# Kernel optimization log

Hardware: AMD Instinct MI355X
Metric: run time of the kernel (lower is better)

Reference implementation:

```python
import jax, jax.numpy as jnp
import numpy as np

NX, NY = 512, 512
DX, DY = 1e-4, 1e-4
VS = 1550.0
DT = 2.5e-8


def setup_inputs() -> dict:
    key = jax.random.key(0)
    k1, k2 = jax.random.split(key)
    sensor_data = jax.random.normal(k1, (4, 2, 128, 2048), dtype=jnp.float32)
    sensor_xy = jax.random.randint(k2, (128, 2), 0, 512, dtype=jnp.int32)
    return {"sensor_data": sensor_data, "sensor_xy": sensor_xy}


def _delay_indices(sensor_xy):
    # pixel grids, 1-indexed as in the torch code (arange(1,513))
    ix = jnp.arange(1, NX + 1, dtype=jnp.float32)[None, :, None]  # (1,Nx,1)
    iy = jnp.arange(1, NY + 1, dtype=jnp.float32)[None, None, :]  # (1,1,Ny)
    x = sensor_xy[:, 0].astype(jnp.float32)[:, None, None]        # (S,1,1)
    y = sensor_xy[:, 1].astype(jnp.float32)[:, None, None]
    dis = jnp.sqrt(((x - ix + 1.0) * DX) ** 2 + ((y - iy + 1.0) * DY) ** 2)  # (S,Nx,Ny)
    # .to(torch.long) truncates; values are non-negative so int cast matches
    return (dis / VS / DT).astype(jnp.int32).reshape(sensor_xy.shape[0], -1)  # (S, Nx*Ny)


def reference(sensor_data, sensor_xy):
    B = sensor_data.shape[0]
    S = sensor_xy.shape[0]
    t = _delay_indices(sensor_xy)                           # (S, P) int32
    data = jnp.transpose(sensor_data, (2, 0, 1, 3))         # (S, B, 2, T)

    def step(img, xs):
        t_s, d_s = xs                                       # (P,), (B,2,T)
        return img + d_s[:, :, t_s], None                   # gather + accumulate

    img0 = jnp.zeros((B, 2, NX * NY), dtype=sensor_data.dtype)
    img, _ = jax.lax.scan(step, img0, (t, data))
    return img.reshape(B, 2, NX, NY)
```

## Files before the change

kernel.cpp:

```cpp
#include <hip/hip_runtime.h>
#include <math.h>


#define NXY 512
#define S_CNT 128
#define T_CNT 2048
#define CH 8
#define CH_STRIDE (S_CNT * T_CNT)
#define NPIX (NXY * NXY)
#define TAB_BYTES (NPIX * 2)
#define CHUNK 32
#define NCHUNK (S_CNT / CHUNK)
#define PATW 24
#define PAT_ROW_B (PATW * 2)
#define PAT_SENS_B (16 * PAT_ROW_B)

typedef float f32x2 __attribute__((ext_vector_type(2)));

#if __has_builtin(__builtin_amdgcn_sad_u32)
__device__ __forceinline__ unsigned int sadu(unsigned int a, unsigned int b, unsigned int c) {
    return __builtin_amdgcn_sad_u32(a, b, c);
}
#else
__device__ __forceinline__ unsigned int sadu(unsigned int a, unsigned int b, unsigned int c) {
    return (a > b ? a - b : b - a) + c;
}
#endif

#pragma float_control(push)
#pragma float_control(precise, on)
__device__ __forceinline__ unsigned short delay_entry(int adx, int ady) {
    const double DX32 = (double)1e-4f;
    const double R1 = (double)(float)(1.0 / 1550.0);
    const double R2 = (double)(float)(1.0 / (double)2.5e-8f);
    float dxf = (float)((double)adx * DX32);
    float dyf = (float)((double)ady * DX32);
    float a2 = (float)((double)dxf * (double)dxf);
    float b2 = (float)((double)dyf * (double)dyf);
    float sum = (float)((double)a2 + (double)b2);
    float dis = (float)sqrt((double)sum);
    float q1 = (float)((double)dis * R1);
    float q2 = (float)((double)q1 * R2);
    return (unsigned short)(int)q2;
}

__device__ __forceinline__ unsigned int bf16_rne(float f) {
    unsigned int x = __float_as_uint(f);
    return (x + 0x7fffu + ((x >> 16) & 1u)) >> 16;
}

__global__ __launch_bounds__(256) void prep(const float* __restrict__ data,
                                            unsigned short* __restrict__ tab,
                                            uint4* __restrict__ d2b) {
    int idx = blockIdx.x * 256 + threadIdx.x;
    tab[idx] = (unsigned short)((unsigned int)delay_entry(idx >> 9, idx & 511) << 4);

    unsigned int w[4];
#pragma unroll
    for (int j = 0; j < 4; ++j) {
        unsigned int lo = bf16_rne(data[(2 * j) * CH_STRIDE + idx]);
        unsigned int hi = bf16_rne(data[(2 * j + 1) * CH_STRIDE + idx]);
        w[j] = lo | (hi << 16);
    }
    d2b[idx] = make_uint4(w[0], w[1], w[2], w[3]);
}
#pragma float_control(pop)

__device__ __forceinline__ float bflo(unsigned int u) { return __uint_as_float(u << 16); }
__device__ __forceinline__ float bfhi(unsigned int u) { return __uint_as_float(u & 0xffff0000u); }

__global__ __launch_bounds__(256) void das_sad(const uint4* __restrict__ d2b,
                                               const unsigned short* __restrict__ tab,
                                               const int* __restrict__ sxy,
                                               float* __restrict__ out) {
    __shared__ uint4 minfo[S_CNT];
    __shared__ unsigned int mstage[S_CNT];
    __shared__ uint4 patb[CHUNK * 16 * 3];

    int tid = threadIdx.x;
    int x0 = (blockIdx.x >> 5) << 4;
    int y0 = (blockIdx.x & 31) << 4;

    if (tid < S_CNT) {
        int sxv = sxy[2 * tid];
        int syv = sxy[2 * tid + 1];
        int axm = sxv < x0 ? x0 - sxv : (sxv > x0 + 15 ? sxv - x0 - 15 : 0);
        int aym = syv < y0 ? y0 - syv : (syv > y0 + 15 ? syv - y0 - 15 : 0);
        int ay0 = aym & ~7;
        minfo[tid] = make_uint4((unsigned int)sxv, (unsigned int)(2 * syv),
                                (unsigned int)(-(axm * 48 + ay0 * 2)), 0u);
        mstage[tid] = (unsigned int)(axm | (ay0 << 16));
    }
    __syncthreads();

    int iy = y0 | (((tid >> 6) & 1) << 3) | (tid & 7);
    int ix = x0 | ((tid >> 7) << 3) | ((tid >> 3) & 7);
    unsigned int uix = (unsigned int)ix;
    unsigned int uiy2 = (unsigned int)(2 * iy);

    f32x2 acc2[4];
#pragma unroll
    for (int k = 0; k < 4; ++k) acc2[k] = (f32x2){0.0f, 0.0f};

    const char* patc = (const char*)patb;

    for (int c = 0; c < NCHUNK; ++c) {
        int s0 = c * CHUNK;

#pragma unroll
        for (int j = 0; j < 6; ++j) {
            unsigned int idx = (unsigned int)tid + 256u * j;
            unsigned int r3 = idx / 3u;
            unsigned int cc = idx - r3 * 3u;
            unsigned int row = r3 & 15u;
            unsigned int ls = r3 >> 4;
            unsigned int st = mstage[s0 + ls];
            int ax0 = (int)(st & 0xffffu);
            int ay0 = (int)(st >> 16);
            const uint4* src = (const uint4*)((const char*)tab +
                (((size_t)(ax0 + (int)row) << 10) + ((size_t)ay0 << 1) + ((size_t)cc << 4)));
            patb[ls * 48u + row * 3u + cc] = *src;
        }
        __syncthreads();

        const char* d2bc = (const char*)d2b + ((size_t)s0 << 15);
#pragma unroll 8
        for (int ls = 0; ls < CHUNK; ++ls) {
            uint4 mi = minfo[s0 + ls];
            unsigned int b1 = sadu(mi.x, uix, 0u);
            unsigned int b2 = sadu(mi.y, uiy2, mi.z);
            unsigned int byte = b1 * 48u + b2;
            unsigned int t16 = (unsigned int)*(const unsigned short*)(
                patc + (size_t)(ls * PAT_SENS_B) + byte);
            uint4 w = *(const uint4*)(d2bc + ((size_t)ls << 15) + t16);
            f32x2 p0 = {bflo(w.x), bfhi(w.x)};
            f32x2 p1 = {bflo(w.y), bfhi(w.y)};
            f32x2 p2 = {bflo(w.z), bfhi(w.z)};
            f32x2 p3 = {bflo(w.w), bfhi(w.w)};
            acc2[0] += p0;
            acc2[1] += p1;
            acc2[2] += p2;
            acc2[3] += p3;
        }
        __syncthreads();
    }

    int pix = (ix << 9) | iy;
#pragma unroll
    for (int k = 0; k < 4; ++k) {
        out[(2 * k) * NPIX + pix] = acc2[k].x;
        out[(2 * k + 1) * NPIX + pix] = acc2[k].y;
    }
}

#pragma float_control(push)
#pragma float_control(precise, on)
__global__ __launch_bounds__(256) void build_table(unsigned short* __restrict__ tab) {
    int idx = blockIdx.x * 256 + threadIdx.x;
    tab[idx] = delay_entry(idx >> 9, idx & 511);
}
#pragma float_control(pop)

__global__ __launch_bounds__(256) void das_main(const float* __restrict__ data,
                                                const unsigned short* __restrict__ tab,
                                                const int* __restrict__ sxy,
                                                float* __restrict__ out) {
    __shared__ int sx[S_CNT];
    __shared__ int sy[S_CNT];
    int tid = threadIdx.x;
    if (tid < S_CNT) {
        sx[tid] = sxy[2 * tid];
        sy[tid] = sxy[2 * tid + 1];
    }
    __syncthreads();
    int iy = ((blockIdx.x & 31) << 4) | (tid & 15);
    int ix = ((blockIdx.x >> 5) << 4) | (tid >> 4);
    float acc[CH];
#pragma unroll
    for (int k = 0; k < CH; ++k) acc[k] = 0.0f;
#pragma unroll 4
    for (int s = 0; s < S_CNT; ++s) {
        int dxi = sx[s] - ix;
        int dyi = sy[s] - iy;
        int adx = dxi < 0 ? -dxi : dxi;
        int ady = dyi < 0 ? -dyi : dyi;
        int t = (int)tab[(adx << 9) | ady];
        const float* p = data + (s << 11) + t;
#pragma unroll
        for (int k = 0; k < CH; ++k) acc[k] += p[(size_t)k * CH_STRIDE];
    }
    int pix = (ix << 9) | iy;
#pragma unroll
    for (int k = 0; k < CH; ++k) out[k * NPIX + pix] = acc[k];
}

extern "C" void kernel_launch(void* const* d_in, const int* in_sizes, int n_in,
                              void* d_out, int out_size, void* d_ws, size_t ws_size,
                              hipStream_t stream) {
    const float* data = (const float*)d_in[0];
    const int* sxy = (const int*)d_in[1];
    float* out = (float*)d_out;
    unsigned short* tab = (unsigned short*)d_ws;

    size_t need = (size_t)TAB_BYTES + (size_t)CH_STRIDE * 16;
    if (ws_size >= need) {
        uint4* d2b = (uint4*)((char*)d_ws + TAB_BYTES);
        prep<<<NPIX / 256, 256, 0, stream>>>(data, tab, d2b);
        das_sad<<<1024, 256, 0, stream>>>(d2b, tab, sxy, out);
    } else {
        build_table<<<NPIX / 256, 256, 0, stream>>>(tab);
        das_main<<<1024, 256, 0, stream>>>(data, tab, sxy, out);
    }
}
```

Baseline: 111.6 us.

## Stage per-sensor time windows in LDS and gather from shared memory

For each 16x16 pixel tile and sensor, the kernel computes the minimum delay and copies a 64-sample window of packed bf16 data into shared memory. The delay pattern is rebased relative to that minimum and XOR-swizzled to reduce bank conflicts. The per-pixel gathers then read from LDS instead of global memory, with table lookups batched ahead of the loads. The chunk size drops from 32 to 8 sensors, which adds more barriers. The code assumes each tile's delay span fits within 64 samples, and the float_control precise pragmas around the delay computation are removed, which could change how the delay indices round.

```diff
diff --git a/kernel.cpp b/kernel.cpp
--- a/kernel.cpp
+++ b/kernel.cpp
@@ -9,8 +9,9 @@
 #define CH_STRIDE (S_CNT * T_CNT)
 #define NPIX (NXY * NXY)
 #define TAB_BYTES (NPIX * 2)
-#define CHUNK 32
+#define CHUNK 8
 #define NCHUNK (S_CNT / CHUNK)
+#define WIN 64
 #define PATW 24
 #define PAT_ROW_B (PATW * 2)
 #define PAT_SENS_B (16 * PAT_ROW_B)
@@ -27,8 +28,6 @@
 }
 #endif
 
-#pragma float_control(push)
-#pragma float_control(precise, on)
 __device__ __forceinline__ unsigned short delay_entry(int adx, int ady) {
     const double DX32 = (double)1e-4f;
     const double R1 = (double)(float)(1.0 / 1550.0);
@@ -64,17 +63,26 @@
     }
     d2b[idx] = make_uint4(w[0], w[1], w[2], w[3]);
 }
-#pragma float_control(pop)
 
 __device__ __forceinline__ float bflo(unsigned int u) { return __uint_as_float(u << 16); }
 __device__ __forceinline__ float bfhi(unsigned int u) { return __uint_as_float(u & 0xffff0000u); }
 
-__global__ __launch_bounds__(256) void das_sad(const uint4* __restrict__ d2b,
+__device__ __forceinline__ unsigned int swz16(unsigned int d) {
+    return d ^ (((d >> 7) & 3u) << 4);
+}
+__device__ __forceinline__ unsigned int subswz_x2(unsigned int a, unsigned int tm4) {
+    unsigned int lo = swz16((a - tm4) & 0xffffu);
+    unsigned int hi = swz16(((a >> 16) - tm4) & 0xffffu);
+    return lo | (hi << 16);
+}
+
+__global__ __launch_bounds__(256) void das_win(const uint4* __restrict__ d2b,
                                                const unsigned short* __restrict__ tab,
                                                const int* __restrict__ sxy,
                                                float* __restrict__ out) {
     __shared__ uint4 minfo[S_CNT];
-    __shared__ unsigned int mstage[S_CNT];
+    __shared__ uint2 mstage[S_CNT];
+    __shared__ uint4 winb[CHUNK * WIN];
     __shared__ uint4 patb[CHUNK * 16 * 3];
 
     int tid = threadIdx.x;
@@ -87,9 +95,11 @@
         int axm = sxv < x0 ? x0 - sxv : (sxv > x0 + 15 ? sxv - x0 - 15 : 0);
         int aym = syv < y0 ? y0 - syv : (syv > y0 + 15 ? syv - y0 - 15 : 0);
         int ay0 = aym & ~7;
+        int tmin = (int)delay_entry(axm, aym);
         minfo[tid] = make_uint4((unsigned int)sxv, (unsigned int)(2 * syv),
                                 (unsigned int)(-(axm * 48 + ay0 * 2)), 0u);
-        mstage[tid] = (unsigned int)(axm | (ay0 << 16));
+        mstage[tid] = make_uint2((unsigned int)(axm | (ay0 << 16)),
+                                 (unsigned int)(tmin << 4));
     }
     __syncthreads();
 
@@ -102,37 +112,62 @@
 #pragma unroll
     for (int k = 0; k < 4; ++k) acc2[k] = (f32x2){0.0f, 0.0f};
 
-    const char* patc = (const char*)patb;
+    char* winc = (char*)winb;
+    char* patc = (char*)patb;
 
     for (int c = 0; c < NCHUNK; ++c) {
         int s0 = c * CHUNK;
 
-#pragma unroll
-        for (int j = 0; j < 6; ++j) {
+        {
+            int lsw = tid >> 5;
+            int e0 = tid & 31;
+            uint2 st = mstage[s0 + lsw];
+            const uint4* src = d2b + ((size_t)(s0 + lsw) << 11) + (st.y >> 4) + e0;
+            unsigned int sw = (((unsigned int)e0 >> 3) & 3u) << 4;
+            unsigned int slot = ((unsigned int)lsw << 10) | (((unsigned int)e0 << 4) ^ sw);
+            uint4 v0 = src[0];
+            uint4 v1 = src[32];
+            *(uint4*)(winc + slot) = v0;
+            *(uint4*)(winc + slot + 512u) = v1;
+        }
+
+#pragma unroll
+        for (int j = 0; j < 2; ++j) {
             unsigned int idx = (unsigned int)tid + 256u * j;
-            unsigned int r3 = idx / 3u;
-            unsigned int cc = idx - r3 * 3u;
-            unsigned int row = r3 & 15u;
-            unsigned int ls = r3 >> 4;
-            unsigned int st = mstage[s0 + ls];
-            int ax0 = (int)(st & 0xffffu);
-            int ay0 = (int)(st >> 16);
-            const uint4* src = (const uint4*)((const char*)tab +
-                (((size_t)(ax0 + (int)row) << 10) + ((size_t)ay0 << 1) + ((size_t)cc << 4)));
-            patb[ls * 48u + row * 3u + cc] = *src;
+            if (idx < 384u) {
+                unsigned int r3 = idx / 3u;
+                unsigned int cc = idx - r3 * 3u;
+                unsigned int row = r3 & 15u;
+                unsigned int ls = r3 >> 4;
+                uint2 st = mstage[s0 + ls];
+                int ax0 = (int)(st.x & 0xffffu);
+                int ay0 = (int)(st.x >> 16);
+                unsigned int tm4 = st.y;
+                uint4 v = *(const uint4*)((const char*)tab +
+                    (((size_t)(ax0 + (int)row) << 10) + ((size_t)ay0 << 1) + ((size_t)cc << 4)));
+                v.x = subswz_x2(v.x, tm4);
+                v.y = subswz_x2(v.y, tm4);
+                v.z = subswz_x2(v.z, tm4);
+                v.w = subswz_x2(v.w, tm4);
+                patb[ls * 48u + row * 3u + cc] = v;
+            }
         }
         __syncthreads();
 
-        const char* d2bc = (const char*)d2b + ((size_t)s0 << 15);
-#pragma unroll 8
-        for (int ls = 0; ls < CHUNK; ++ls) {
-            uint4 mi = minfo[s0 + ls];
+        unsigned int t16[CHUNK];
+#pragma unroll
+        for (int j = 0; j < CHUNK; ++j) {
+            uint4 mi = minfo[s0 + j];
             unsigned int b1 = sadu(mi.x, uix, 0u);
             unsigned int b2 = sadu(mi.y, uiy2, mi.z);
             unsigned int byte = b1 * 48u + b2;
-            unsigned int t16 = (unsigned int)*(const unsigned short*)(
-                patc + (size_t)(ls * PAT_SENS_B) + byte);
-            uint4 w = *(const uint4*)(d2bc + ((size_t)ls << 15) + t16);
+            t16[j] = (unsigned int)*(const unsigned short*)(
+                patc + (unsigned int)(j * PAT_SENS_B) + byte);
+        }
+
+#pragma unroll
+        for (int j = 0; j < CHUNK; ++j) {
+            uint4 w = *(const uint4*)(winc + (unsigned int)(j << 10) + t16[j]);
             f32x2 p0 = {bflo(w.x), bfhi(w.x)};
             f32x2 p1 = {bflo(w.y), bfhi(w.y)};
             f32x2 p2 = {bflo(w.z), bfhi(w.z)};
@@ -153,13 +188,10 @@
     }
 }
 
-#pragma float_control(push)
-#pragma float_control(precise, on)
 __global__ __launch_bounds__(256) void build_table(unsigned short* __restrict__ tab) {
     int idx = blockIdx.x * 256 + threadIdx.x;
     tab[idx] = delay_entry(idx >> 9, idx & 511);
 }
-#pragma float_control(pop)
 
 __global__ __launch_bounds__(256) void das_main(const float* __restrict__ data,
                                                 const unsigned short* __restrict__ tab,
@@ -206,7 +238,7 @@
     if (ws_size >= need) {
         uint4* d2b = (uint4*)((char*)d_ws + TAB_BYTES);
         prep<<<NPIX / 256, 256, 0, stream>>>(data, tab, d2b);
-        das_sad<<<1024, 256, 0, stream>>>(d2b, tab, sxy, out);
+        das_win<<<1024, 256, 0, stream>>>(d2b, tab, sxy, out);
     } else {
         build_table<<<NPIX / 256, 256, 0, stream>>>(tab);
         das_main<<<1024, 256, 0, stream>>>(data, tab, sxy, out);
```

Result: faster. 101.5 us (-9.0%).
